# Kernel optimization log

Hardware: AMD Instinct MI355X
Metric: run time of the kernel (lower is better)

The kernel has to match this reference:

```python
import jax, jax.numpy as jnp
import numpy as np

V, D, L, H, FF, S = 32000, 400, 6, 8, 1600, 2048
B, N = 2, 2048
HD = D // H


def setup_inputs() -> dict:
    key = jax.random.key(0)
    ks = jax.random.split(key, 9)
    n = lambda k, shape: 0.02 * jax.random.normal(k, shape, dtype=jnp.float32)
    return {
        "idx": jax.random.randint(ks[0], (B, N), 0, V),
        "tok_emb": n(ks[1], (V, D)),
        "pos_emb": n(ks[2], (S, D)),
        "ln1_w": jnp.ones((L, D), jnp.float32), "ln1_b": jnp.zeros((L, D), jnp.float32),
        "qkv_w": n(ks[3], (L, D, 3 * D)), "qkv_b": jnp.zeros((L, 3 * D), jnp.float32),
        "attn_out_w": n(ks[4], (L, D, D)), "attn_out_b": jnp.zeros((L, D), jnp.float32),
        "ln2_w": jnp.ones((L, D), jnp.float32), "ln2_b": jnp.zeros((L, D), jnp.float32),
        "fc1_w": n(ks[5], (L, D, FF)), "fc1_b": jnp.zeros((L, FF), jnp.float32),
        "fc2_w": n(ks[6], (L, FF, D)), "fc2_b": jnp.zeros((L, D), jnp.float32),
        "lnf_w": jnp.ones((D,), jnp.float32), "lnf_b": jnp.zeros((D,), jnp.float32),
        "head_w": n(ks[7], (D, V)),
    }


def _ln(x, w, b):
    m = x.mean(-1, keepdims=True)
    v = ((x - m) ** 2).mean(-1, keepdims=True)
    return (x - m) * jax.lax.rsqrt(v + 1e-5) * w + b


def reference(idx, tok_emb, pos_emb, ln1_w, ln1_b, qkv_w, qkv_b, attn_out_w, attn_out_b,
              ln2_w, ln2_b, fc1_w, fc1_b, fc2_w, fc2_b, lnf_w, lnf_b, head_w):
    b, n = idx.shape
    scale = HD ** -0.5
    x = tok_emb[idx] + pos_emb[None, :n]          # [B,N,D]
    mask = jnp.tril(jnp.ones((n, n), dtype=bool))  # causal mask
    for l in range(L):
        h = _ln(x, ln1_w[l], ln1_b[l])
        qkv = h @ qkv_w[l] + qkv_b[l]
        q, k, v = jnp.split(qkv, 3, axis=-1)
        q = q.reshape(b, n, H, HD)
        k = k.reshape(b, n, H, HD)
        v = v.reshape(b, n, H, HD)
        s = jnp.einsum('bihd,bjhd->bhij', q, k) * scale   # [B,H,N,N]
        s = jnp.where(mask, s, -jnp.inf)
        a = jax.nn.softmax(s, axis=-1)
        o = jnp.einsum('bhij,bjhd->bihd', a, v).reshape(b, n, D)
        x = x + o @ attn_out_w[l] + attn_out_b[l]
        h = _ln(x, ln2_w[l], ln2_b[l])
        x = x + jax.nn.gelu(h @ fc1_w[l] + fc1_b[l], approximate=False) @ fc2_w[l] + fc2_b[l]
    return _ln(x, lnf_w, lnf_b) @ head_w          # [B,N,V] logits
```

## Files before the change

### kernel.cpp

```cpp
#include <hip/hip_runtime.h>
#include <hip/hip_bf16.h>
#include <math.h>

constexpr int V  = 32000;
constexpr int D  = 400;
constexpr int L  = 6;
constexpr int H  = 8;
constexpr int FF = 1600;
constexpr int B  = 2;
constexpr int N  = 2048;
constexpr int HD = D / H;
constexpr int TD = 3 * D;
constexpr int M  = B * N;
constexpr int KP = 416;

typedef __bf16 bf16x8 __attribute__((ext_vector_type(8)));
typedef float  f32x4  __attribute__((ext_vector_type(4)));
typedef unsigned short us16x4 __attribute__((ext_vector_type(4)));

static __device__ __forceinline__ float wave_sum_f(float v) {
#pragma unroll
    for (int m = 32; m; m >>= 1) v += __shfl_xor(v, m, 64);
    return v;
}

static __device__ __forceinline__ void gl_lds16(const unsigned short* g, unsigned short* l) {
    __builtin_amdgcn_global_load_lds(
        (const __attribute__((address_space(1))) unsigned int*)(g),
        (__attribute__((address_space(3))) unsigned int*)(l), 16, 0, 0);
}

static __device__ __forceinline__ unsigned short f2bf(float f) {
    __hip_bfloat16 h = __float2bfloat16(f);
    return *reinterpret_cast<unsigned short*>(&h);
}

__global__ __launch_bounds__(256) void embed_kernel(const int* __restrict__ idx,
                                                    const float* __restrict__ tok,
                                                    const float* __restrict__ pos,
                                                    float* __restrict__ x) {
    size_t i = (size_t)blockIdx.x * 256 + threadIdx.x;
    if (i >= (size_t)M * D) return;
    int d  = (int)(i % D);
    int bn = (int)(i / D);
    int n  = bn % N;
    x[i] = tok[(size_t)idx[bn] * D + d] + pos[(size_t)n * D + d];
}

__global__ __launch_bounds__(256) void wconv_kernel(const float* __restrict__ W,
                                                    __hip_bfloat16* __restrict__ Bt,
                                                    int K, int Nw, int Kp, int Nr,
                                                    long sW, long sBt) {
    const int l = blockIdx.z;
    __shared__ float t[32][33];
    const int k0 = blockIdx.x * 32, n0 = blockIdx.y * 32;
    const float* Wl = W + (size_t)l * sW;
    __hip_bfloat16* Btl = Bt + (size_t)l * sBt;
    for (int i = 0; i < 32; i += 8) {
        int k = k0 + threadIdx.y + i, n = n0 + threadIdx.x;
        t[threadIdx.y + i][threadIdx.x] = (k < K && n < Nw) ? Wl[(size_t)k * Nw + n] : 0.f;
    }
    __syncthreads();
    for (int i = 0; i < 32; i += 8) {
        int n = n0 + threadIdx.y + i, k = k0 + threadIdx.x;
        if (n < Nr && k < Kp) Btl[(size_t)n * Kp + k] = __float2bfloat16(t[threadIdx.x][threadIdx.y + i]);
    }
}

__global__ __launch_bounds__(256) void ln_bf16_kernel(const float* __restrict__ in,
                                                      const float* __restrict__ w,
                                                      const float* __restrict__ b,
                                                      __hip_bfloat16* __restrict__ out) {
    const int row  = blockIdx.x * 4 + (threadIdx.x >> 6);
    const int lane = threadIdx.x & 63;
    const float* xr = in + (size_t)row * D;
    float s = 0.f, ss = 0.f;
    for (int d = lane; d < D; d += 64) {
        float v = xr[d];
        s += v; ss += v * v;
    }
    s  = wave_sum_f(s);
    ss = wave_sum_f(ss);
    float mean = s * (1.0f / D);
    float var  = ss * (1.0f / D) - mean * mean;
    float rstd = rsqrtf(var + 1e-5f);
    __hip_bfloat16* orow = out + (size_t)row * KP;
    for (int d = lane; d < KP; d += 64)
        orow[d] = __float2bfloat16(d < D ? (xr[d] - mean) * rstd * w[d] + b[d] : 0.f);
}

template <bool BIAS, bool RES, bool GELU, bool OUTBF, bool SWAPXY = false>
__global__ __launch_bounds__(256) void mm_kernel(const unsigned short* __restrict__ A,
                                                 const unsigned short* __restrict__ Bt,
                                                 const float* __restrict__ bias,
                                                 const float* __restrict__ res,
                                                 void* __restrict__ Cv,
                                                 int Nc, int Kp) {
    __shared__ __align__(1024) unsigned short As[128 * 32];
    __shared__ __align__(1024) unsigned short Bs[128 * 32];
    const int tid  = threadIdx.x;
    const int lane = tid & 63, wid = tid >> 6;
    const int wr = wid >> 1, wc = wid & 1;
    const int bx = SWAPXY ? blockIdx.y : blockIdx.x;
    const int by = SWAPXY ? blockIdx.x : blockIdx.y;

    f32x4 acc[4][4] = {};

    const unsigned short* Abase = A  + (size_t)(by * 128) * Kp;
    const unsigned short* Bbase = Bt + (size_t)(bx * 128) * Kp;
    const int lrow = lane >> 2;
    const int lcol = (lane & 3) * 8;

    for (int k0 = 0; k0 < Kp; k0 += 32) {
#pragma unroll
        for (int c = 0; c < 2; ++c) {
            const int chunk = wid * 2 + c;
            gl_lds16(Abase + (size_t)(chunk * 16 + lrow) * Kp + k0 + lcol, As + chunk * 512);
            gl_lds16(Bbase + (size_t)(chunk * 16 + lrow) * Kp + k0 + lcol, Bs + chunk * 512);
        }
        __syncthreads();
        bf16x8 a[4], b[4];
#pragma unroll
        for (int m = 0; m < 4; ++m)
            a[m] = *(const bf16x8*)(As + (wr * 64 + m * 16 + (lane & 15)) * 32 + (lane >> 4) * 8);
#pragma unroll
        for (int n = 0; n < 4; ++n)
            b[n] = *(const bf16x8*)(Bs + (wc * 64 + n * 16 + (lane & 15)) * 32 + (lane >> 4) * 8);
#pragma unroll
        for (int m = 0; m < 4; ++m)
#pragma unroll
            for (int n = 0; n < 4; ++n)
                acc[m][n] = __builtin_amdgcn_mfma_f32_16x16x32_bf16(a[m], b[n], acc[m][n], 0, 0, 0);
        __syncthreads();
    }

    const int col_base = bx * 128 + wc * 64 + (lane & 15);
    const int row_base = by * 128 + wr * 64 + ((lane >> 4) << 2);
#pragma unroll
    for (int n = 0; n < 4; ++n) {
        const int col = col_base + n * 16;
        if (col >= Nc) continue;
        const float bv = BIAS ? bias[col] : 0.f;
#pragma unroll
        for (int m = 0; m < 4; ++m) {
#pragma unroll
            for (int r = 0; r < 4; ++r) {
                const int row = row_base + m * 16 + r;
                float v = acc[m][n][r] + bv;
                if (GELU) v = 0.5f * v * (1.0f + erff(v * 0.70710678118654752f));
                const size_t ci = (size_t)row * Nc + col;
                if (RES) v += res[ci];
                if (OUTBF) ((__hip_bfloat16*)Cv)[ci] = __float2bfloat16(v);
                else       ((float*)Cv)[ci] = v;
            }
        }
    }
}

template <bool BIAS, bool RES, bool GELU, bool OUTBF>
__global__ __launch_bounds__(256) void mm64_kernel(const unsigned short* __restrict__ A,
                                                   const unsigned short* __restrict__ Bt,
                                                   const float* __restrict__ bias,
                                                   const float* __restrict__ res,
                                                   void* __restrict__ Cv,
                                                   int Nc, int Kp) {
    __shared__ __align__(1024) unsigned short As[64 * 32];
    __shared__ __align__(1024) unsigned short Bs[128 * 32];
    const int tid  = threadIdx.x;
    const int lane = tid & 63, wid = tid >> 6;
    const int wr = wid >> 1, wc = wid & 1;
    const int bx = blockIdx.x, by = blockIdx.y;
    const int l15 = lane & 15, g = lane >> 4;

    f32x4 acc[2][4] = {};

    const unsigned short* Abase = A  + (size_t)(by * 64) * Kp;
    const unsigned short* Bbase = Bt + (size_t)(bx * 128) * Kp;
    const int lrow = lane >> 2;
    const int lcol = (lane & 3) * 8;

    for (int k0 = 0; k0 < Kp; k0 += 32) {
        gl_lds16(Abase + (size_t)(wid * 16 + lrow) * Kp + k0 + lcol, As + wid * 512);
#pragma unroll
        for (int c = 0; c < 2; ++c) {
            const int chunk = wid * 2 + c;
            gl_lds16(Bbase + (size_t)(chunk * 16 + lrow) * Kp + k0 + lcol, Bs + chunk * 512);
        }
        __syncthreads();
        bf16x8 a[2], b[4];
#pragma unroll
        for (int m = 0; m < 2; ++m)
            a[m] = *(const bf16x8*)(As + (wr * 32 + m * 16 + l15) * 32 + g * 8);
#pragma unroll
        for (int n = 0; n < 4; ++n)
            b[n] = *(const bf16x8*)(Bs + (wc * 64 + n * 16 + l15) * 32 + g * 8);
#pragma unroll
        for (int m = 0; m < 2; ++m)
#pragma unroll
            for (int n = 0; n < 4; ++n)
                acc[m][n] = __builtin_amdgcn_mfma_f32_16x16x32_bf16(a[m], b[n], acc[m][n], 0, 0, 0);
        __syncthreads();
    }

    const int col_base = bx * 128 + wc * 64 + l15;
    const int row_base = by * 64 + wr * 32 + (g << 2);
#pragma unroll
    for (int n = 0; n < 4; ++n) {
        const int col = col_base + n * 16;
        if (col >= Nc) continue;
        const float bv = BIAS ? bias[col] : 0.f;
#pragma unroll
        for (int m = 0; m < 2; ++m) {
#pragma unroll
            for (int r = 0; r < 4; ++r) {
                const int row = row_base + m * 16 + r;
                float v = acc[m][n][r] + bv;
                if (GELU) v = 0.5f * v * (1.0f + erff(v * 0.70710678118654752f));
                const size_t ci = (size_t)row * Nc + col;
                if (RES) v += res[ci];
                if (OUTBF) ((__hip_bfloat16*)Cv)[ci] = __float2bfloat16(v);
                else       ((float*)Cv)[ci] = v;
            }
        }
    }
}

__global__ __launch_bounds__(256) void mm_qkv_kernel(const unsigned short* __restrict__ A,
                                                     const unsigned short* __restrict__ Bt,
                                                     const float* __restrict__ bias,
                                                     unsigned short* __restrict__ Qb,
                                                     unsigned short* __restrict__ Kb,
                                                     unsigned short* __restrict__ Vt) {
    __shared__ __align__(1024) unsigned short As[128 * 32];
    __shared__ __align__(1024) unsigned short Bs[128 * 32];
    const int tid  = threadIdx.x;
    const int lane = tid & 63, wid = tid >> 6;
    const int wr = wid >> 1, wc = wid & 1;
    const int bx = blockIdx.x, by = blockIdx.y;

    f32x4 acc[4][4] = {};

    const unsigned short* Abase = A  + (size_t)(by * 128) * KP;
    const unsigned short* Bbase = Bt + (size_t)(bx * 128) * KP;
    const int lrow = lane >> 2;
    const int lcol = (lane & 3) * 8;

    for (int k0 = 0; k0 < KP; k0 += 32) {
#pragma unroll
        for (int c = 0; c < 2; ++c) {
            const int chunk = wid * 2 + c;
            gl_lds16(Abase + (size_t)(chunk * 16 + lrow) * KP + k0 + lcol, As + chunk * 512);
            gl_lds16(Bbase + (size_t)(chunk * 16 + lrow) * KP + k0 + lcol, Bs + chunk * 512);
        }
        __syncthreads();
        bf16x8 a[4], b[4];
#pragma unroll
        for (int m = 0; m < 4; ++m)
            a[m] = *(const bf16x8*)(As + (wr * 64 + m * 16 + (lane & 15)) * 32 + (lane >> 4) * 8);
#pragma unroll
        for (int n = 0; n < 4; ++n)
            b[n] = *(const bf16x8*)(Bs + (wc * 64 + n * 16 + (lane & 15)) * 32 + (lane >> 4) * 8);
#pragma unroll
        for (int m = 0; m < 4; ++m)
#pragma unroll
            for (int n = 0; n < 4; ++n)
                acc[m][n] = __builtin_amdgcn_mfma_f32_16x16x32_bf16(a[m], b[n], acc[m][n], 0, 0, 0);
        __syncthreads();
    }

    const float scale = 0.14142135623730950f;
    const int col_base = bx * 128 + wc * 64 + (lane & 15);
    const int row_base = by * 128 + wr * 64 + ((lane >> 4) << 2);
#pragma unroll
    for (int n = 0; n < 4; ++n) {
        const int col = col_base + n * 16;
        if (col >= TD) continue;
        const int part = col < D ? 0 : (col < 2 * D ? 1 : 2);
        const int cc = col - part * D;
        const int h = cc / HD, d = cc % HD;
        const float bv = bias[col];
#pragma unroll
        for (int m = 0; m < 4; ++m) {
            const int row0 = row_base + m * 16;
            const int b = row0 >> 11, nn0 = row0 & (N - 1);
            const int bh = b * H + h;
            if (part == 2) {
                us16x4 pk;
#pragma unroll
                for (int r = 0; r < 4; ++r) pk[r] = f2bf(acc[m][n][r] + bv);
                *(us16x4*)(Vt + (size_t)(bh * 64 + d) * N + nn0) = pk;
            } else if (part == 0) {
#pragma unroll
                for (int r = 0; r < 4; ++r)
                    Qb[(size_t)(bh * N + nn0 + r) * 64 + d] = f2bf((acc[m][n][r] + bv) * scale);
            } else {
#pragma unroll
                for (int r = 0; r < 4; ++r)
                    Kb[(size_t)(bh * N + nn0 + r) * 64 + d] = f2bf(acc[m][n][r] + bv);
            }
        }
    }
}

__global__ __launch_bounds__(256) void fattn_kernel(const unsigned short* __restrict__ Qb,
                                                    const unsigned short* __restrict__ Kb,
                                                    const unsigned short* __restrict__ Vt,
                                                    __hip_bfloat16* __restrict__ o) {
    const int q0 = blockIdx.x * 64, h = blockIdx.y, b = blockIdx.z;
    const int bh = b * H + h;
    const int tid = threadIdx.x, lane = tid & 63, w = tid >> 6;
    const int l15 = lane & 15, g = lane >> 4;

    __shared__ __align__(1024) unsigned short Ks[2][64 * 64];
    __shared__ __align__(1024) unsigned short Vs[2][64 * 64];
    __shared__ __hip_bfloat16 P_s[4][16 * 72];
    unsigned short* Pw = (unsigned short*)&P_s[w][0];

    const int st_r    = (lane >> 3);
    const int st_cblk = (lane ^ (lane >> 3)) & 7;

    const unsigned short* Qrow = Qb + ((size_t)(bh * N + q0 + w * 16 + l15)) * 64 + g * 8;
    const bf16x8 qa0 = *(const bf16x8*)(Qrow);
    const bf16x8 qa1 = *(const bf16x8*)(Qrow + 32);

    f32x4 acc[4] = {};
    float ssum[4] = {0.f, 0.f, 0.f, 0.f};

    const int nt = q0 / 64 + 1;

#define STAGE(buf, j0)                                                                     \
    {                                                                                      \
        _Pragma("unroll")                                                                  \
        for (int c = 0; c < 2; ++c) {                                                      \
            const int rr = (w * 2 + c) * 8 + st_r;                                         \
            gl_lds16(Kb + (size_t)(bh * N + (j0) + rr) * 64 + st_cblk * 8,                 \
                     &Ks[buf][(w * 2 + c) * 512]);                                         \
            gl_lds16(Vt + (size_t)(bh * 64 + rr) * N + (j0) + st_cblk * 8,                 \
                     &Vs[buf][(w * 2 + c) * 512]);                                         \
        }                                                                                  \
    }

    STAGE(0, 0);
    __syncthreads();

    for (int t = 0; t < nt; ++t) {
        const int cur = t & 1;
        if (t + 1 < nt) STAGE(cur ^ 1, (t + 1) * 64);

        f32x4 s[4];
        const int swz = ((l15 & 7) << 3);
#pragma unroll
        for (int n = 0; n < 4; ++n) {
            const unsigned short* kbase = &Ks[cur][(n * 16 + l15) * 64];
            bf16x8 k0 = *(const bf16x8*)(kbase + ((g * 8) ^ swz));
            bf16x8 k1 = *(const bf16x8*)(kbase + (((g + 4) * 8) ^ swz));
            f32x4 z = {};
            z    = __builtin_amdgcn_mfma_f32_16x16x32_bf16(qa0, k0, z, 0, 0, 0);
            s[n] = __builtin_amdgcn_mfma_f32_16x16x32_bf16(qa1, k1, z, 0, 0, 0);
        }
        if (t == nt - 1) {
#pragma unroll
            for (int n = 0; n < 4; ++n)
#pragma unroll
                for (int r = 0; r < 4; ++r)
                    if (l15 + n * 16 > w * 16 + g * 4 + r) s[n][r] = -INFINITY;
        }
#pragma unroll
        for (int n = 0; n < 4; ++n)
#pragma unroll
            for (int r = 0; r < 4; ++r) {
                float p = __expf(s[n][r]);
                ssum[r] += p;
                Pw[(g * 4 + r) * 72 + l15 + n * 16] = f2bf(p);
            }
        bf16x8 pa0 = *(const bf16x8*)(Pw + l15 * 72 + g * 8);
        bf16x8 pa1 = *(const bf16x8*)(Pw + l15 * 72 + 32 + g * 8);

#pragma unroll
        for (int n = 0; n < 4; ++n) {
            const unsigned short* vbase = &Vs[cur][(n * 16 + l15) * 64];
            bf16x8 v0 = *(const bf16x8*)(vbase + ((g * 8) ^ swz));
            bf16x8 v1 = *(const bf16x8*)(vbase + (((g + 4) * 8) ^ swz));
            acc[n] = __builtin_amdgcn_mfma_f32_16x16x32_bf16(pa0, v0, acc[n], 0, 0, 0);
            acc[n] = __builtin_amdgcn_mfma_f32_16x16x32_bf16(pa1, v1, acc[n], 0, 0, 0);
        }

        __syncthreads();
    }
#undef STAGE

#pragma unroll
    for (int r = 0; r < 4; ++r)
#pragma unroll
        for (int msk = 1; msk < 16; msk <<= 1) ssum[r] += __shfl_xor(ssum[r], msk, 64);

#pragma unroll
    for (int n = 0; n < 4; ++n) {
        const int d = n * 16 + l15;
        if (d < HD) {
#pragma unroll
            for (int r = 0; r < 4; ++r) {
                const int row = b * N + q0 + w * 16 + g * 4 + r;
                o[(size_t)row * KP + h * HD + d] = __float2bfloat16(acc[n][r] / ssum[r]);
            }
        }
    }
}

extern "C" void kernel_launch(void* const* d_in, const int* in_sizes, int n_in,
                              void* d_out, int out_size, void* d_ws, size_t ws_size,
                              hipStream_t stream) {
    const int*   idx        = (const int*)d_in[0];
    const float* tok_emb    = (const float*)d_in[1];
    const float* pos_emb    = (const float*)d_in[2];
    const float* ln1_w      = (const float*)d_in[3];
    const float* ln1_b      = (const float*)d_in[4];
    const float* qkv_w      = (const float*)d_in[5];
    const float* qkv_b      = (const float*)d_in[6];
    const float* attn_out_w = (const float*)d_in[7];
    const float* attn_out_b = (const float*)d_in[8];
    const float* ln2_w      = (const float*)d_in[9];
    const float* ln2_b      = (const float*)d_in[10];
    const float* fc1_w      = (const float*)d_in[11];
    const float* fc1_b      = (const float*)d_in[12];
    const float* fc2_w      = (const float*)d_in[13];
    const float* fc2_b      = (const float*)d_in[14];
    const float* lnf_w      = (const float*)d_in[15];
    const float* lnf_b      = (const float*)d_in[16];
    const float* head_w     = (const float*)d_in[17];
    float* out = (float*)d_out;

    char* ws = (char*)d_ws;
    __hip_bfloat16* hb   = (__hip_bfloat16*)(ws);
    float*          x    = (float*)(ws + 3407872);
    __hip_bfloat16* ff   = (__hip_bfloat16*)(ws + 9961472);
    __hip_bfloat16* ob   = (__hip_bfloat16*)(ws + 23068672);
    __hip_bfloat16* headt = (__hip_bfloat16*)(ws + 3407872);

    char* wout = (char*)d_out;
    __hip_bfloat16* qkvt = (__hip_bfloat16*)(wout);
    __hip_bfloat16* aot  = (__hip_bfloat16*)(wout + 6389760);
    __hip_bfloat16* fc1t = (__hip_bfloat16*)(wout + 8945664);
    __hip_bfloat16* fc2t = (__hip_bfloat16*)(wout + 17252352);
    unsigned short* qb_g = (unsigned short*)(wout + 27082752);
    unsigned short* kb_g = (unsigned short*)(wout + 31277056);
    unsigned short* vt_g = (unsigned short*)(wout + 35471360);

    const dim3 tb(32, 8);
    wconv_kernel<<<dim3(13, 40, L), tb, 0, stream>>>(qkv_w,      qkvt, D,  TD, KP, 1280, (long)D * TD, 1280L * KP);
    wconv_kernel<<<dim3(13, 16, L), tb, 0, stream>>>(attn_out_w, aot,  D,  D,  KP, 512,  (long)D * D,  512L * KP);
    wconv_kernel<<<dim3(13, 52, L), tb, 0, stream>>>(fc1_w,      fc1t, D,  FF, KP, 1664, (long)D * FF, 1664L * KP);
    wconv_kernel<<<dim3(50, 16, L), tb, 0, stream>>>(fc2_w,      fc2t, FF, D,  FF, 512,  (long)FF * D, 512L * (long)FF);

    embed_kernel<<<dim3((M * D + 255) / 256), dim3(256), 0, stream>>>(idx, tok_emb, pos_emb, x);
    hipMemsetAsync(ob, 0, (size_t)M * KP * sizeof(__hip_bfloat16), stream);
    hipMemsetAsync(qb_g, 0, 3 * 4194304, stream);

    for (int l = 0; l < L; ++l) {
        ln_bf16_kernel<<<dim3(M / 4), dim3(256), 0, stream>>>(x, ln1_w + (size_t)l * D, ln1_b + (size_t)l * D, hb);
        mm_qkv_kernel<<<dim3(10, 32), dim3(256), 0, stream>>>(
            (const unsigned short*)hb, (const unsigned short*)(qkvt + (size_t)l * 1280 * KP),
            qkv_b + (size_t)l * TD, qb_g, kb_g, vt_g);
        fattn_kernel<<<dim3(N / 64, H, B), dim3(256), 0, stream>>>(qb_g, kb_g, vt_g, ob);
        mm64_kernel<true, true, false, false><<<dim3(4, 64), dim3(256), 0, stream>>>(
            (const unsigned short*)ob, (const unsigned short*)(aot + (size_t)l * 512 * KP),
            attn_out_b + (size_t)l * D, x, x, D, KP);
        ln_bf16_kernel<<<dim3(M / 4), dim3(256), 0, stream>>>(x, ln2_w + (size_t)l * D, ln2_b + (size_t)l * D, hb);
        mm_kernel<true, false, true, true><<<dim3(13, 32), dim3(256), 0, stream>>>(
            (const unsigned short*)hb, (const unsigned short*)(fc1t + (size_t)l * 1664 * KP),
            fc1_b + (size_t)l * FF, nullptr, ff, FF, KP);
        mm64_kernel<true, true, false, false><<<dim3(4, 64), dim3(256), 0, stream>>>(
            (const unsigned short*)ff, (const unsigned short*)(fc2t + (size_t)l * 512 * FF),
            fc2_b + (size_t)l * D, x, x, D, FF);
    }

    ln_bf16_kernel<<<dim3(M / 4), dim3(256), 0, stream>>>(x, lnf_w, lnf_b, hb);
    wconv_kernel<<<dim3(13, 1000, 1), tb, 0, stream>>>(head_w, headt, D, V, KP, V, 0, 0);
    mm_kernel<false, false, false, false, true><<<dim3(M / 128, V / 128), dim3(256), 0, stream>>>(
        (const unsigned short*)hb, (const unsigned short*)headt, nullptr, nullptr, out, V, KP);
}
```

Before: 1.148 ms.

## Fuse LayerNorm into residual GEMM epilogues and embedding kernel

Replaces the standalone LayerNorm kernels by computing row statistics inside the attention-out and fc2 GEMM epilogues and inside the embedding kernel. The new GEMM uses 16-row tiles spanning all output columns so each block owns full rows for the reduction. This removes separate launches and extra reads of the residual stream. The trade-off is more repeated weight loading per block and less MFMA reuse per loaded A tile.

```diff
diff --git a/kernel.cpp b/kernel.cpp
--- a/kernel.cpp
+++ b/kernel.cpp
@@ -35,16 +35,47 @@
     return *reinterpret_cast<unsigned short*>(&h);
 }
 
-__global__ __launch_bounds__(256) void embed_kernel(const int* __restrict__ idx,
-                                                    const float* __restrict__ tok,
-                                                    const float* __restrict__ pos,
-                                                    float* __restrict__ x) {
-    size_t i = (size_t)blockIdx.x * 256 + threadIdx.x;
-    if (i >= (size_t)M * D) return;
-    int d  = (int)(i % D);
-    int bn = (int)(i / D);
-    int n  = bn % N;
-    x[i] = tok[(size_t)idx[bn] * D + d] + pos[(size_t)n * D + d];
+__global__ __launch_bounds__(256) void embed_ln_kernel(const int* __restrict__ idx,
+                                                       const float* __restrict__ tok,
+                                                       const float* __restrict__ pos,
+                                                       const float* __restrict__ lnw,
+                                                       const float* __restrict__ lnb,
+                                                       float* __restrict__ x,
+                                                       __hip_bfloat16* __restrict__ hb) {
+    const int row  = blockIdx.x * 4 + (threadIdx.x >> 6);
+    const int lane = threadIdx.x & 63;
+    const int n = row & (N - 1);
+    const float* tr = tok + (size_t)idx[row] * D;
+    const float* pr = pos + (size_t)n * D;
+
+    float v[7];
+    float s = 0.f, ss = 0.f;
+#pragma unroll
+    for (int i = 0; i < 7; ++i) {
+        const int d = lane + i * 64;
+        if (d < D) {
+            v[i] = tr[d] + pr[d];
+            s += v[i]; ss += v[i] * v[i];
+        } else v[i] = 0.f;
+    }
+    s  = wave_sum_f(s);
+    ss = wave_sum_f(ss);
+    const float mean = s * (1.0f / D);
+    const float var  = ss * (1.0f / D) - mean * mean;
+    const float rstd = rsqrtf(var + 1e-5f);
+
+    float* xr = x + (size_t)row * D;
+    __hip_bfloat16* hr = hb + (size_t)row * KP;
+#pragma unroll
+    for (int i = 0; i < 7; ++i) {
+        const int d = lane + i * 64;
+        if (d < D) {
+            xr[d] = v[i];
+            hr[d] = __float2bfloat16((v[i] - mean) * rstd * lnw[d] + lnb[d]);
+        } else if (d < KP) {
+            hr[d] = __float2bfloat16(0.f);
+        }
+    }
 }
 
 __global__ __launch_bounds__(256) void wconv_kernel(const float* __restrict__ W,
@@ -65,28 +96,6 @@
         int n = n0 + threadIdx.y + i, k = k0 + threadIdx.x;
         if (n < Nr && k < Kp) Btl[(size_t)n * Kp + k] = __float2bfloat16(t[threadIdx.x][threadIdx.y + i]);
     }
-}
-
-__global__ __launch_bounds__(256) void ln_bf16_kernel(const float* __restrict__ in,
-                                                      const float* __restrict__ w,
-                                                      const float* __restrict__ b,
-                                                      __hip_bfloat16* __restrict__ out) {
-    const int row  = blockIdx.x * 4 + (threadIdx.x >> 6);
-    const int lane = threadIdx.x & 63;
-    const float* xr = in + (size_t)row * D;
-    float s = 0.f, ss = 0.f;
-    for (int d = lane; d < D; d += 64) {
-        float v = xr[d];
-        s += v; ss += v * v;
-    }
-    s  = wave_sum_f(s);
-    ss = wave_sum_f(ss);
-    float mean = s * (1.0f / D);
-    float var  = ss * (1.0f / D) - mean * mean;
-    float rstd = rsqrtf(var + 1e-5f);
-    __hip_bfloat16* orow = out + (size_t)row * KP;
-    for (int d = lane; d < KP; d += 64)
-        orow[d] = __float2bfloat16(d < D ? (xr[d] - mean) * rstd * w[d] + b[d] : 0.f);
 }
 
 template <bool BIAS, bool RES, bool GELU, bool OUTBF, bool SWAPXY = false>
@@ -157,70 +166,102 @@
     }
 }
 
-template <bool BIAS, bool RES, bool GELU, bool OUTBF>
-__global__ __launch_bounds__(256) void mm64_kernel(const unsigned short* __restrict__ A,
-                                                   const unsigned short* __restrict__ Bt,
-                                                   const float* __restrict__ bias,
-                                                   const float* __restrict__ res,
-                                                   void* __restrict__ Cv,
-                                                   int Nc, int Kp) {
-    __shared__ __align__(1024) unsigned short As[64 * 32];
-    __shared__ __align__(1024) unsigned short Bs[128 * 32];
+__global__ __launch_bounds__(256) void mmfuse_kernel(const unsigned short* __restrict__ A,
+                                                     const unsigned short* __restrict__ Bt,
+                                                     const float* __restrict__ bias,
+                                                     const float* __restrict__ lnw,
+                                                     const float* __restrict__ lnb,
+                                                     float* __restrict__ x,
+                                                     __hip_bfloat16* __restrict__ hb,
+                                                     int Kp) {
+    __shared__ __align__(1024) unsigned short As[16 * 32];
+    __shared__ __align__(1024) unsigned short Bs[512 * 32];
+    __shared__ float red[4][16][2];
     const int tid  = threadIdx.x;
     const int lane = tid & 63, wid = tid >> 6;
-    const int wr = wid >> 1, wc = wid & 1;
-    const int bx = blockIdx.x, by = blockIdx.y;
     const int l15 = lane & 15, g = lane >> 4;
-
-    f32x4 acc[2][4] = {};
-
-    const unsigned short* Abase = A  + (size_t)(by * 64) * Kp;
-    const unsigned short* Bbase = Bt + (size_t)(bx * 128) * Kp;
+    const int by = blockIdx.x;
+
+    f32x4 acc[8] = {};
+
+    const unsigned short* Abase = A + (size_t)(by * 16) * Kp;
     const int lrow = lane >> 2;
     const int lcol = (lane & 3) * 8;
 
     for (int k0 = 0; k0 < Kp; k0 += 32) {
-        gl_lds16(Abase + (size_t)(wid * 16 + lrow) * Kp + k0 + lcol, As + wid * 512);
-#pragma unroll
-        for (int c = 0; c < 2; ++c) {
-            const int chunk = wid * 2 + c;
-            gl_lds16(Bbase + (size_t)(chunk * 16 + lrow) * Kp + k0 + lcol, Bs + chunk * 512);
-        }
-        __syncthreads();
-        bf16x8 a[2], b[4];
-#pragma unroll
-        for (int m = 0; m < 2; ++m)
-            a[m] = *(const bf16x8*)(As + (wr * 32 + m * 16 + l15) * 32 + g * 8);
-#pragma unroll
-        for (int n = 0; n < 4; ++n)
-            b[n] = *(const bf16x8*)(Bs + (wc * 64 + n * 16 + l15) * 32 + g * 8);
-#pragma unroll
-        for (int m = 0; m < 2; ++m)
-#pragma unroll
-            for (int n = 0; n < 4; ++n)
-                acc[m][n] = __builtin_amdgcn_mfma_f32_16x16x32_bf16(a[m], b[n], acc[m][n], 0, 0, 0);
-        __syncthreads();
-    }
-
-    const int col_base = bx * 128 + wc * 64 + l15;
-    const int row_base = by * 64 + wr * 32 + (g << 2);
-#pragma unroll
-    for (int n = 0; n < 4; ++n) {
-        const int col = col_base + n * 16;
-        if (col >= Nc) continue;
-        const float bv = BIAS ? bias[col] : 0.f;
-#pragma unroll
-        for (int m = 0; m < 2; ++m) {
-#pragma unroll
-            for (int r = 0; r < 4; ++r) {
-                const int row = row_base + m * 16 + r;
-                float v = acc[m][n][r] + bv;
-                if (GELU) v = 0.5f * v * (1.0f + erff(v * 0.70710678118654752f));
-                const size_t ci = (size_t)row * Nc + col;
-                if (RES) v += res[ci];
-                if (OUTBF) ((__hip_bfloat16*)Cv)[ci] = __float2bfloat16(v);
-                else       ((float*)Cv)[ci] = v;
-            }
+        if (wid == 0)
+            gl_lds16(Abase + (size_t)lrow * Kp + k0 + lcol, As);
+#pragma unroll
+        for (int c = 0; c < 8; ++c) {
+            const int chunk = wid * 8 + c;
+            gl_lds16(Bt + (size_t)(chunk * 16 + lrow) * Kp + k0 + lcol, Bs + chunk * 512);
+        }
+        __syncthreads();
+        const bf16x8 a = *(const bf16x8*)(As + l15 * 32 + g * 8);
+#pragma unroll
+        for (int n = 0; n < 8; ++n) {
+            const bf16x8 b = *(const bf16x8*)(Bs + (wid * 128 + n * 16 + l15) * 32 + g * 8);
+            acc[n] = __builtin_amdgcn_mfma_f32_16x16x32_bf16(a, b, acc[n], 0, 0, 0);
+        }
+        __syncthreads();
+    }
+
+    float ps[4] = {0.f, 0.f, 0.f, 0.f}, pss[4] = {0.f, 0.f, 0.f, 0.f};
+#pragma unroll
+    for (int n = 0; n < 8; ++n) {
+        const int col = wid * 128 + n * 16 + l15;
+        const bool ok = col < D;
+        const float bv = ok ? bias[col] : 0.f;
+#pragma unroll
+        for (int r = 0; r < 4; ++r) {
+            const int rowl = g * 4 + r;
+            float v = 0.f;
+            if (ok) v = acc[n][r] + bv + x[(size_t)(by * 16 + rowl) * D + col];
+            acc[n][r] = v;
+            ps[r] += v; pss[r] += v * v;
+        }
+    }
+#pragma unroll
+    for (int r = 0; r < 4; ++r) {
+#pragma unroll
+        for (int msk = 1; msk < 16; msk <<= 1) {
+            ps[r]  += __shfl_xor(ps[r],  msk, 64);
+            pss[r] += __shfl_xor(pss[r], msk, 64);
+        }
+    }
+    if (l15 == 0) {
+#pragma unroll
+        for (int r = 0; r < 4; ++r) {
+            red[wid][g * 4 + r][0] = ps[r];
+            red[wid][g * 4 + r][1] = pss[r];
+        }
+    }
+    __syncthreads();
+
+    float mean[4], rstd[4];
+#pragma unroll
+    for (int r = 0; r < 4; ++r) {
+        const int rowl = g * 4 + r;
+        const float s  = red[0][rowl][0] + red[1][rowl][0] + red[2][rowl][0] + red[3][rowl][0];
+        const float ss = red[0][rowl][1] + red[1][rowl][1] + red[2][rowl][1] + red[3][rowl][1];
+        mean[r] = s * (1.0f / D);
+        const float var = ss * (1.0f / D) - mean[r] * mean[r];
+        rstd[r] = rsqrtf(var + 1e-5f);
+    }
+
+#pragma unroll
+    for (int n = 0; n < 8; ++n) {
+        const int col = wid * 128 + n * 16 + l15;
+        if (col >= KP) continue;
+        const bool ok = col < D;
+        const float w = ok ? lnw[col] : 0.f;
+        const float bb = ok ? lnb[col] : 0.f;
+#pragma unroll
+        for (int r = 0; r < 4; ++r) {
+            const int row = by * 16 + g * 4 + r;
+            if (ok) x[(size_t)row * D + col] = acc[n][r];
+            const float h = ok ? (acc[n][r] - mean[r]) * rstd[r] * w + bb : 0.f;
+            hb[(size_t)row * KP + col] = __float2bfloat16(h);
         }
     }
 }
@@ -452,29 +493,28 @@
     wconv_kernel<<<dim3(13, 52, L), tb, 0, stream>>>(fc1_w,      fc1t, D,  FF, KP, 1664, (long)D * FF, 1664L * KP);
     wconv_kernel<<<dim3(50, 16, L), tb, 0, stream>>>(fc2_w,      fc2t, FF, D,  FF, 512,  (long)FF * D, 512L * (long)FF);
 
-    embed_kernel<<<dim3((M * D + 255) / 256), dim3(256), 0, stream>>>(idx, tok_emb, pos_emb, x);
+    embed_ln_kernel<<<dim3(M / 4), dim3(256), 0, stream>>>(idx, tok_emb, pos_emb, ln1_w, ln1_b, x, hb);
     hipMemsetAsync(ob, 0, (size_t)M * KP * sizeof(__hip_bfloat16), stream);
     hipMemsetAsync(qb_g, 0, 3 * 4194304, stream);
 
     for (int l = 0; l < L; ++l) {
-        ln_bf16_kernel<<<dim3(M / 4), dim3(256), 0, stream>>>(x, ln1_w + (size_t)l * D, ln1_b + (size_t)l * D, hb);
         mm_qkv_kernel<<<dim3(10, 32), dim3(256), 0, stream>>>(
             (const unsigned short*)hb, (const unsigned short*)(qkvt + (size_t)l * 1280 * KP),
             qkv_b + (size_t)l * TD, qb_g, kb_g, vt_g);
         fattn_kernel<<<dim3(N / 64, H, B), dim3(256), 0, stream>>>(qb_g, kb_g, vt_g, ob);
-        mm64_kernel<true, true, false, false><<<dim3(4, 64), dim3(256), 0, stream>>>(
+        mmfuse_kernel<<<dim3(M / 16), dim3(256), 0, stream>>>(
             (const unsigned short*)ob, (const unsigned short*)(aot + (size_t)l * 512 * KP),
-            attn_out_b + (size_t)l * D, x, x, D, KP);
-        ln_bf16_kernel<<<dim3(M / 4), dim3(256), 0, stream>>>(x, ln2_w + (size_t)l * D, ln2_b + (size_t)l * D, hb);
+            attn_out_b + (size_t)l * D, ln2_w + (size_t)l * D, ln2_b + (size_t)l * D, x, hb, KP);
         mm_kernel<true, false, true, true><<<dim3(13, 32), dim3(256), 0, stream>>>(
             (const unsigned short*)hb, (const unsigned short*)(fc1t + (size_t)l * 1664 * KP),
             fc1_b + (size_t)l * FF, nullptr, ff, FF, KP);
-        mm64_kernel<true, true, false, false><<<dim3(4, 64), dim3(256), 0, stream>>>(
+        const float* nw = (l < L - 1) ? ln1_w + (size_t)(l + 1) * D : lnf_w;
+        const float* nb = (l < L - 1) ? ln1_b + (size_t)(l + 1) * D : lnf_b;
+        mmfuse_kernel<<<dim3(M / 16), dim3(256), 0, stream>>>(
             (const unsigned short*)ff, (const unsigned short*)(fc2t + (size_t)l * 512 * FF),
-            fc2_b + (size_t)l * D, x, x, D, FF);
-    }
-
-    ln_bf16_kernel<<<dim3(M / 4), dim3(256), 0, stream>>>(x, lnf_w, lnf_b, hb);
+            fc2_b + (size_t)l * D, nw, nb, x, hb, FF);
+    }
+
     wconv_kernel<<<dim3(13, 1000, 1), tb, 0, stream>>>(head_w, headt, D, V, KP, V, 0, 0);
     mm_kernel<false, false, false, false, true><<<dim3(M / 128, V / 128), dim3(256), 0, stream>>>(
         (const unsigned short*)hb, (const unsigned short*)headt, nullptr, nullptr, out, V, KP);
```

Measured after the change: 1.347 ms. 17.4% more time.
